# Performance work log

Measured on AMD Instinct MI355X. Metric: run time of the kernel, lower is better.

## Reference

```python
import jax, jax.numpy as jnp
import numpy as np

N_USER = 50000
N_ITEM = 50000
E = 500000
D_IN = 256
H = 4
D_HID = 64
D_OUT = 128
NEG_SLOPE = 0.2  # DGL GATConv default leaky_relu slope


def setup_inputs() -> dict:
    key = jax.random.key(0)
    ks = jax.random.split(key, 14)
    f = lambda k, s: jax.random.normal(k, s, dtype=jnp.float32)
    return {
        "h_src_user": f(ks[0], (N_USER, D_IN)),
        "h_src_item": f(ks[1], (N_ITEM, D_IN)),
        "h_dst_user": f(ks[2], (N_USER, D_IN)),
        "h_dst_item": f(ks[3], (N_ITEM, D_IN)),
        "u2i_src": jax.random.randint(ks[4], (E,), 0, N_USER),
        "u2i_dst": jax.random.randint(ks[5], (E,), 0, N_ITEM),
        "i2u_src": jax.random.randint(ks[6], (E,), 0, N_ITEM),
        "i2u_dst": jax.random.randint(ks[7], (E,), 0, N_USER),
        "fc_w": f(ks[8], (D_IN, H * D_HID)) * 0.05,
        "attn_l": f(ks[9], (H, D_HID)) * 0.05,
        "attn_r": f(ks[10], (H, D_HID)) * 0.05,
        "gat_bias": jnp.zeros((H * D_HID,), jnp.float32),
        "W_w": f(ks[11], (D_IN + D_HID, D_OUT)) * 0.05,
        "W_b": jnp.zeros((D_OUT,), jnp.float32),
    }


def _gat(feat_src, feat_dst, src, dst, n_dst, fc_w, attn_l, attn_r, gat_bias):
    # DGL GATConv (dropout is identity in eval mode)
    H_, D_ = attn_l.shape
    fs = (feat_src @ fc_w).reshape(-1, H_, D_)  # [Ns,H,D]
    fd = (feat_dst @ fc_w).reshape(-1, H_, D_)  # [Nd,H,D]
    el = jnp.sum(fs * attn_l, axis=-1)          # [Ns,H]
    er = jnp.sum(fd * attn_r, axis=-1)          # [Nd,H]
    e = jax.nn.leaky_relu(el[src] + er[dst], NEG_SLOPE)  # [E,H]
    # edge softmax per (dst node, head)
    m = jax.ops.segment_max(e, dst, num_segments=n_dst)
    m = jnp.where(jnp.isfinite(m), m, 0.0)      # guard zero-degree dst
    ex = jnp.exp(e - m[dst])
    den = jax.ops.segment_sum(ex, dst, num_segments=n_dst)
    alpha = ex / jnp.where(den == 0, 1.0, den)[dst]      # [E,H]
    out = jax.ops.segment_sum(alpha[:, :, None] * fs[src], dst, num_segments=n_dst)
    return out + gat_bias.reshape(1, H_, D_)    # [Nd,H,D]


def _head(agg, h_dst, W_w, W_b):
    # mean over heads, concat with dst feats, linear+relu, safe L2 normalize
    z = jax.nn.relu(jnp.concatenate([agg.mean(axis=1), h_dst], axis=1) @ W_w + W_b)
    n = jnp.linalg.norm(z, axis=1, keepdims=True)
    return z / jnp.where(n == 0, 1.0, n)


def reference(h_src_user, h_src_item, h_dst_user, h_dst_item,
              u2i_src, u2i_dst, i2u_src, i2u_dst,
              fc_w, attn_l, attn_r, gat_bias, W_w, W_b):
    agg_item = _gat(h_src_user, h_dst_item, u2i_src, u2i_dst, N_ITEM, fc_w, attn_l, attn_r, gat_bias)
    agg_user = _gat(h_src_item, h_dst_user, i2u_src, i2u_dst, N_USER, fc_w, attn_l, attn_r, gat_bias)
    z_user = _head(agg_user, h_dst_user, W_w, W_b)
    z_item = _head(agg_item, h_dst_item, W_w, W_b)
    return z_user, z_item
```

## Files before the change

kernel.cpp:

```cpp
#include <hip/hip_runtime.h>

#define NN 50000
#define N2 100000
#define EE 500000
#define E2 1000000

typedef unsigned short u16;
typedef unsigned int u32;

typedef __attribute__((ext_vector_type(8))) __bf16 bf16x8;
typedef __attribute__((ext_vector_type(4))) float f32x4;

__device__ __forceinline__ float4 ld4(const float* p) { return *(const float4*)p; }

__device__ __forceinline__ u16 f2bf(float f) {
  u32 u = __float_as_uint(f);
  u += 0x7FFFu + ((u >> 16) & 1u);
  return (u16)(u >> 16);
}

__device__ __forceinline__ u32 cvtpk(float lo, float hi) {
  u32 r;
  asm("v_cvt_pk_bf16_f32 %0, %1, %2" : "=v"(r) : "v"(lo), "v"(hi));
  return r;
}

__global__ void L384_const(const float* fc_w, const float* attn_l,
                           const float* attn_r, const float* Ww, float* w_r,
                           u16* wlB, u16* Bt, u16* Wt, int* cur) {
  const int b = blockIdx.x;
  const int t = threadIdx.x;
  if (b < 256) {
    Bt[b * 256 + t] = f2bf(fc_w[(size_t)t * 256 + b]);
  } else if (b == 256) {
    for (int h = 0; h < 4; ++h) {
      float sl = 0.f, sr = 0.f;
      for (int d = 0; d < 64; ++d) {
        float f = fc_w[t * 256 + h * 64 + d];
        sl += f * attn_l[h * 64 + d];
        sr += f * attn_r[h * 64 + d];
      }
      w_r[t * 4 + h] = sr;
      wlB[h * 256 + t] = f2bf(sl);
    }
    for (int h = 4; h < 16; ++h) wlB[h * 256 + t] = 0;
  } else if (b < 385) {
    int n = b - 257;
    for (int k = t; k < 320; k += 256)
      Wt[(size_t)n * 320 + k] = f2bf(Ww[(size_t)k * 128 + n]);
  } else {
    int i = (b - 385) * 256 + t;
    if (i < N2) cur[i] = 0;
  }
}

__global__ void L384_prep(const float* Du, const float* Di, const float* w_r_,
                          u16* X, float* er, const int* i2u_dst,
                          const int* u2i_dst, int* cnt) {
  const int b = blockIdx.x;
  if (b >= 25000) {
    int e = (b - 25000) * 256 + threadIdx.x;
    if (e < EE) {
      int d = i2u_dst[e];
      d = ((unsigned)d < NN) ? d : 0;
      atomicAdd(&cnt[d], 1);
    } else if (e < E2) {
      int d = u2i_dst[e - EE];
      d = ((unsigned)d < NN) ? d : 0;
      atomicAdd(&cnt[NN + d], 1);
    }
    return;
  }
  const int r = b * 4 + (threadIdx.x >> 6);
  const int lane = threadIdx.x & 63;
  if (r >= N2) return;
  const float* src = (r < NN) ? Du + (size_t)r * 256 : Di + (size_t)(r - NN) * 256;
  float4 xv = ld4(src + lane * 4);
  uint2 pk = make_uint2(cvtpk(xv.x, xv.y), cvtpk(xv.z, xv.w));
  *(uint2*)(X + (size_t)r * 320 + 64 + lane * 4) = pk;
  const float* wr = w_r_ + lane * 16;
  float4 w0 = ld4(wr), w1 = ld4(wr + 4), w2 = ld4(wr + 8), w3 = ld4(wr + 12);
  float a0 = xv.x * w0.x + xv.y * w1.x + xv.z * w2.x + xv.w * w3.x;
  float a1 = xv.x * w0.y + xv.y * w1.y + xv.z * w2.y + xv.w * w3.y;
  float a2 = xv.x * w0.z + xv.y * w1.z + xv.z * w2.z + xv.w * w3.z;
  float a3 = xv.x * w0.w + xv.y * w1.w + xv.z * w2.w + xv.w * w3.w;
  for (int off = 32; off; off >>= 1) {
    a0 += __shfl_xor(a0, off);
    a1 += __shfl_xor(a1, off);
    a2 += __shfl_xor(a2, off);
    a3 += __shfl_xor(a3, off);
  }
  if (lane == 0) {
    float* op = er + (size_t)r * 4;
    op[0] = a0; op[1] = a1; op[2] = a2; op[3] = a3;
  }
}

__global__ void L384_scan1(const int* cnt, int* part, int* bsum, int n) {
  __shared__ int sh[256];
  const int t = threadIdx.x;
  const int base = blockIdx.x * 1024 + t * 4;
  int v0 = (base + 0 < n) ? cnt[base + 0] : 0;
  int v1 = (base + 1 < n) ? cnt[base + 1] : 0;
  int v2 = (base + 2 < n) ? cnt[base + 2] : 0;
  int v3 = (base + 3 < n) ? cnt[base + 3] : 0;
  int s0 = v0, s1 = s0 + v1, s2 = s1 + v2, s3 = s2 + v3;
  sh[t] = s3;
  __syncthreads();
  for (int off = 1; off < 256; off <<= 1) {
    int x = (t >= off) ? sh[t - off] : 0;
    __syncthreads();
    sh[t] += x;
    __syncthreads();
  }
  int excl = (t > 0) ? sh[t - 1] : 0;
  if (base + 0 < n) part[base + 0] = excl;
  if (base + 1 < n) part[base + 1] = excl + s0;
  if (base + 2 < n) part[base + 2] = excl + s1;
  if (base + 3 < n) part[base + 3] = excl + s2;
  if (t == 255) bsum[blockIdx.x] = sh[255];
}
__global__ void L384_scan23(int* indptr, const int* bsum, int* cur, int nb, int n) {
  __shared__ int pre[128];
  const int t = threadIdx.x;
  if (t == 0) {
    int acc = 0;
    for (int i = 0; i < nb; ++i) {
      pre[i] = acc;
      acc += bsum[i];
    }
    pre[nb] = acc;
  }
  __syncthreads();
  int i = blockIdx.x * 256 + t;
  if (i < n) {
    int v = indptr[i] + pre[i >> 10];
    indptr[i] = v;
    cur[i] = v;
  }
  if (blockIdx.x == 0 && t == 0) indptr[n] = pre[nb];
}

__global__ __launch_bounds__(512) void L384_gemm(const float* Au, const float* Ai,
                                                 const u16* Bt, const u16* wlB,
                                                 u16* C, float* el,
                                                 const int* i2u_src, const int* i2u_dst,
                                                 const int* u2i_src, const int* u2i_dst,
                                                 int* cur, int* csr) {
  __shared__ u16 bs[64][264];
  const int t = threadIdx.x;
  if (blockIdx.x >= 782) {
    int e = (blockIdx.x - 782) * 512 + t;
    if (e < EE) {
      int d = i2u_dst[e];
      d = ((unsigned)d < NN) ? d : 0;
      int s = i2u_src[e];
      s = ((unsigned)s < NN) ? s : 0;
      int pos = atomicAdd(&cur[d], 1);
      if ((unsigned)pos < E2) csr[pos] = NN + s;
    } else if (e < E2) {
      int d = u2i_dst[e - EE];
      d = ((unsigned)d < NN) ? d : 0;
      int s = u2i_src[e - EE];
      s = ((unsigned)s < NN) ? s : 0;
      int pos = atomicAdd(&cur[NN + d], 1);
      if ((unsigned)pos < E2) csr[pos] = s;
    }
    return;
  }
  const int w = t >> 6;
  const int l = t & 63;
  const int lr = l & 15;
  const int kg = l >> 4;
  const int row0 = blockIdx.x * 128;

  const int row = row0 + w * 16 + lr;
  const int rr = (row < N2) ? row : (N2 - 1);
  const float* arow =
      ((rr < NN) ? Au + (size_t)rr * 256 : Ai + (size_t)(rr - NN) * 256) + kg * 8;
  uint4 a[8];
#pragma unroll
  for (int ks = 0; ks < 8; ++ks) {
    float4 f0 = ld4(arow + ks * 32);
    float4 f1 = ld4(arow + ks * 32 + 4);
    a[ks] = make_uint4(cvtpk(f0.x, f0.y), cvtpk(f0.z, f0.w), cvtpk(f1.x, f1.y),
                       cvtpk(f1.z, f1.w));
  }

  {
    f32x4 eacc = {0.f, 0.f, 0.f, 0.f};
    const u16* wl = wlB + lr * 256 + kg * 8;
#pragma unroll
    for (int ks = 0; ks < 8; ++ks) {
      union { bf16x8 v; uint4 q; } af, wf;
      af.q = a[ks];
      wf.q = *(const uint4*)(wl + ks * 32);
      eacc = __builtin_amdgcn_mfma_f32_16x16x32_bf16(af.v, wf.v, eacc, 0, 0, 0);
    }
    if (lr < 4) {
#pragma unroll
      for (int r = 0; r < 4; ++r) {
        int grow = row0 + w * 16 + kg * 4 + r;
        if (grow < N2) el[(size_t)grow * 4 + lr] = eacc[r];
      }
    }
  }

  for (int strip = 0; strip < 4; ++strip) {
    __syncthreads();
    {
      const int brow = t >> 3;
      const int bc = (t & 7) * 32;
      const uint4* s = (const uint4*)(Bt + (size_t)(strip * 64 + brow) * 256 + bc);
      uint4* d = (uint4*)&bs[brow][bc];
      d[0] = s[0]; d[1] = s[1]; d[2] = s[2]; d[3] = s[3];
    }
    __syncthreads();

    f32x4 acc[4];
#pragma unroll
    for (int ct = 0; ct < 4; ++ct) acc[ct] = (f32x4){0.f, 0.f, 0.f, 0.f};
#pragma unroll
    for (int ks = 0; ks < 8; ++ks) {
      union { bf16x8 v; uint4 q; } af;
      af.q = a[ks];
#pragma unroll
      for (int ct = 0; ct < 4; ++ct) {
        union { bf16x8 v; uint4 q; } b;
        b.q = *(const uint4*)&bs[ct * 16 + lr][ks * 32 + kg * 8];
        acc[ct] = __builtin_amdgcn_mfma_f32_16x16x32_bf16(af.v, b.v, acc[ct], 0, 0, 0);
      }
    }

#pragma unroll
    for (int p = 0; p < 2; ++p) {
      __syncthreads();
      if ((w >> 2) == p) {
        const int lrow = (w & 3) * 16 + kg * 4;
#pragma unroll
        for (int ct = 0; ct < 4; ++ct)
#pragma unroll
          for (int r = 0; r < 4; ++r)
            bs[lrow + r][ct * 16 + lr] = f2bf(acc[ct][r]);
      }
      __syncthreads();
      const int lrow2 = t >> 3;
      const int c0 = (t & 7) * 8;
      const int grow = row0 + p * 64 + lrow2;
      if (grow < N2)
        *(uint4*)(C + (size_t)grow * 256 + strip * 64 + c0) =
            *(const uint4*)&bs[lrow2][c0];
    }
  }
}

__global__ void L384_sort(const int* indptr, int* csr, int n) {
  __shared__ int buf[5120];
  const int t = threadIdx.x;
  const int node0 = blockIdx.x * 256;
  const int nEnd = (node0 + 256 < n) ? (node0 + 256) : n;
  if (node0 >= n) return;
  const int segL = indptr[node0];
  const int segR = indptr[nEnd];
  const int len = segR - segL;
  if (len <= 5120) {
    for (int i = t; i < len; i += 256) buf[i] = csr[segL + i];
    __syncthreads();
    const int node = node0 + t;
    if (node < n) {
      int p0 = indptr[node] - segL;
      int p1 = indptr[node + 1] - segL;
      for (int a = p0 + 1; a < p1; ++a) {
        int v = buf[a];
        int b = a - 1;
        while (b >= p0 && buf[b] > v) {
          buf[b + 1] = buf[b];
          --b;
        }
        buf[b + 1] = v;
      }
    }
    __syncthreads();
    for (int i = t; i < len; i += 256) csr[segL + i] = buf[i];
  } else {
    const int node = node0 + t;
    if (node < n) {
      int p0 = indptr[node], p1 = indptr[node + 1];
      for (int a = p0 + 1; a < p1; ++a) {
        int v = csr[a];
        int b = a - 1;
        while (b >= p0 && csr[b] > v) {
          csr[b + 1] = csr[b];
          --b;
        }
        csr[b + 1] = v;
      }
    }
  }
}

__global__ void L384_aggx(const int* indptr, const int* csr, const float* el,
                          const float* er, const u16* fs, const float* bias,
                          float* alphaG, u16* X) {
  __shared__ float aL[4][64][4];
  __shared__ int sL[4][64];
  const int slot = threadIdx.x >> 6;
  const int wid = blockIdx.x * 4 + slot;
  const int lane = threadIdx.x & 63;
  if (wid >= N2) return;
  const int p0 = indptr[wid];
  const int deg = indptr[wid + 1] - p0;
  const int h = lane >> 4;
  const int c = lane & 15;
  float4 er4 = ld4(er + (size_t)wid * 4);

  const bool small = (deg <= 64);
  if (small) {
    float4 ex = {0.f, 0.f, 0.f, 0.f};
    int s = 0;
    if (lane < deg) {
      s = csr[p0 + lane];
      s = ((unsigned)s < N2) ? s : 0;
      float4 ev = ld4(el + (size_t)s * 4);
      float e0 = ev.x + er4.x; e0 = (e0 >= 0.f) ? e0 : 0.2f * e0;
      float e1 = ev.y + er4.y; e1 = (e1 >= 0.f) ? e1 : 0.2f * e1;
      float e2 = ev.z + er4.z; e2 = (e2 >= 0.f) ? e2 : 0.2f * e2;
      float e3 = ev.w + er4.w; e3 = (e3 >= 0.f) ? e3 : 0.2f * e3;
      ex = make_float4(__expf(e0), __expf(e1), __expf(e2), __expf(e3));
    }
    float d0 = ex.x, d1 = ex.y, d2 = ex.z, d3 = ex.w;
    for (int off = 32; off; off >>= 1) {
      d0 += __shfl_xor(d0, off);
      d1 += __shfl_xor(d1, off);
      d2 += __shfl_xor(d2, off);
      d3 += __shfl_xor(d3, off);
    }
    if (lane < deg) {
      float4 o = make_float4(ex.x / d0, ex.y / d1, ex.z / d2, ex.w / d3);
      *(float4*)&aL[slot][lane][0] = o;
      sL[slot][lane] = s;
    }
  } else if (deg > 0) {
    float d0 = 0.f, d1 = 0.f, d2 = 0.f, d3 = 0.f;
    for (int i = lane; i < deg; i += 64) {
      int s = csr[p0 + i];
      s = ((unsigned)s < N2) ? s : 0;
      float4 ev = ld4(el + (size_t)s * 4);
      float e0 = ev.x + er4.x; e0 = (e0 >= 0.f) ? e0 : 0.2f * e0;
      float e1 = ev.y + er4.y; e1 = (e1 >= 0.f) ? e1 : 0.2f * e1;
      float e2 = ev.z + er4.z; e2 = (e2 >= 0.f) ? e2 : 0.2f * e2;
      float e3 = ev.w + er4.w; e3 = (e3 >= 0.f) ? e3 : 0.2f * e3;
      float4 ex = make_float4(__expf(e0), __expf(e1), __expf(e2), __expf(e3));
      *(float4*)(alphaG + (size_t)(p0 + i) * 4) = ex;
      d0 += ex.x; d1 += ex.y; d2 += ex.z; d3 += ex.w;
    }
    for (int off = 32; off; off >>= 1) {
      d0 += __shfl_xor(d0, off);
      d1 += __shfl_xor(d1, off);
      d2 += __shfl_xor(d2, off);
      d3 += __shfl_xor(d3, off);
    }
    float i0 = 1.f / d0, i1 = 1.f / d1, i2 = 1.f / d2, i3 = 1.f / d3;
    for (int i = lane; i < deg; i += 64) {
      float4 ex = *(const float4*)(alphaG + (size_t)(p0 + i) * 4);
      *(float4*)(alphaG + (size_t)(p0 + i) * 4) =
          make_float4(ex.x * i0, ex.y * i1, ex.z * i2, ex.w * i3);
    }
  }

  float ax = 0.f, ay = 0.f, az = 0.f, aw = 0.f;
  int i = 0;
  for (; i + 4 <= deg; i += 4) {
    int s0, s1, s2, s3;
    float a0, a1, a2, a3;
    if (small) {
      s0 = sL[slot][i + 0]; s1 = sL[slot][i + 1];
      s2 = sL[slot][i + 2]; s3 = sL[slot][i + 3];
      a0 = aL[slot][i + 0][h]; a1 = aL[slot][i + 1][h];
      a2 = aL[slot][i + 2][h]; a3 = aL[slot][i + 3][h];
    } else {
      s0 = csr[p0 + i + 0]; s0 = ((unsigned)s0 < N2) ? s0 : 0;
      s1 = csr[p0 + i + 1]; s1 = ((unsigned)s1 < N2) ? s1 : 0;
      s2 = csr[p0 + i + 2]; s2 = ((unsigned)s2 < N2) ? s2 : 0;
      s3 = csr[p0 + i + 3]; s3 = ((unsigned)s3 < N2) ? s3 : 0;
      a0 = alphaG[(size_t)(p0 + i + 0) * 4 + h];
      a1 = alphaG[(size_t)(p0 + i + 1) * 4 + h];
      a2 = alphaG[(size_t)(p0 + i + 2) * 4 + h];
      a3 = alphaG[(size_t)(p0 + i + 3) * 4 + h];
    }
    uint2 q0 = *(const uint2*)(fs + (size_t)s0 * 256 + lane * 4);
    uint2 q1 = *(const uint2*)(fs + (size_t)s1 * 256 + lane * 4);
    uint2 q2 = *(const uint2*)(fs + (size_t)s2 * 256 + lane * 4);
    uint2 q3 = *(const uint2*)(fs + (size_t)s3 * 256 + lane * 4);
    ax += a0 * __uint_as_float(q0.x << 16);
    ay += a0 * __uint_as_float(q0.x & 0xffff0000u);
    az += a0 * __uint_as_float(q0.y << 16);
    aw += a0 * __uint_as_float(q0.y & 0xffff0000u);
    ax += a1 * __uint_as_float(q1.x << 16);
    ay += a1 * __uint_as_float(q1.x & 0xffff0000u);
    az += a1 * __uint_as_float(q1.y << 16);
    aw += a1 * __uint_as_float(q1.y & 0xffff0000u);
    ax += a2 * __uint_as_float(q2.x << 16);
    ay += a2 * __uint_as_float(q2.x & 0xffff0000u);
    az += a2 * __uint_as_float(q2.y << 16);
    aw += a2 * __uint_as_float(q2.y & 0xffff0000u);
    ax += a3 * __uint_as_float(q3.x << 16);
    ay += a3 * __uint_as_float(q3.x & 0xffff0000u);
    az += a3 * __uint_as_float(q3.y << 16);
    aw += a3 * __uint_as_float(q3.y & 0xffff0000u);
  }
  for (; i < deg; ++i) {
    int s0;
    float a0;
    if (small) {
      s0 = sL[slot][i];
      a0 = aL[slot][i][h];
    } else {
      s0 = csr[p0 + i]; s0 = ((unsigned)s0 < N2) ? s0 : 0;
      a0 = alphaG[(size_t)(p0 + i) * 4 + h];
    }
    uint2 q0 = *(const uint2*)(fs + (size_t)s0 * 256 + lane * 4);
    ax += a0 * __uint_as_float(q0.x << 16);
    ay += a0 * __uint_as_float(q0.x & 0xffff0000u);
    az += a0 * __uint_as_float(q0.y << 16);
    aw += a0 * __uint_as_float(q0.y & 0xffff0000u);
  }
  const float* bp = bias + lane * 4;
  float ox = ax + bp[0];
  float oy = ay + bp[1];
  float oz = az + bp[2];
  float ow = aw + bp[3];
  for (int off = 16; off <= 32; off <<= 1) {
    ox += __shfl_xor(ox, off);
    oy += __shfl_xor(oy, off);
    oz += __shfl_xor(oz, off);
    ow += __shfl_xor(ow, off);
  }
  if (h == 0) {
    uint2 pk = make_uint2(cvtpk(ox * 0.25f, oy * 0.25f), cvtpk(oz * 0.25f, ow * 0.25f));
    *(uint2*)(X + (size_t)wid * 320 + 4 * c) = pk;
  }
}

__global__ void L384_headm(const u16* X, const u16* Wt, const float* Wb, float* out) {
  __shared__ float red[4][64];
  const int t = threadIdx.x;
  const int w = t >> 6;
  const int l = t & 63;
  const int row0 = blockIdx.x * 64;
  const int lr = l & 15;
  const int kg = l >> 4;
  f32x4 acc[4][2];
#pragma unroll
  for (int rg = 0; rg < 4; ++rg) {
    acc[rg][0] = (f32x4){0.f, 0.f, 0.f, 0.f};
    acc[rg][1] = (f32x4){0.f, 0.f, 0.f, 0.f};
  }
  const u16* arow[4];
#pragma unroll
  for (int rg = 0; rg < 4; ++rg) {
    int r = row0 + rg * 16 + lr;
    if (r >= N2) r = N2 - 1;
    arow[rg] = X + (size_t)r * 320 + kg * 8;
  }
  const u16* b0row = Wt + (size_t)(w * 32 + lr) * 320 + kg * 8;
  const u16* b1row = Wt + (size_t)(w * 32 + 16 + lr) * 320 + kg * 8;
#pragma unroll
  for (int k0 = 0; k0 < 320; k0 += 32) {
    union { bf16x8 v; uint4 q; } af[4], b0, b1;
#pragma unroll
    for (int rg = 0; rg < 4; ++rg) af[rg].q = *(const uint4*)(arow[rg] + k0);
    b0.q = *(const uint4*)(b0row + k0);
    b1.q = *(const uint4*)(b1row + k0);
#pragma unroll
    for (int rg = 0; rg < 4; ++rg) {
      acc[rg][0] = __builtin_amdgcn_mfma_f32_16x16x32_bf16(af[rg].v, b0.v,
                                                           acc[rg][0], 0, 0, 0);
      acc[rg][1] = __builtin_amdgcn_mfma_f32_16x16x32_bf16(af[rg].v, b1.v,
                                                           acc[rg][1], 0, 0, 0);
    }
  }
  const int col0 = w * 32 + lr;
  const int col1 = col0 + 16;
  float wb0 = Wb[col0], wb1 = Wb[col1];
  float z0[4][4], z1[4][4];
#pragma unroll
  for (int rg = 0; rg < 4; ++rg) {
    float pssq[4];
#pragma unroll
    for (int r = 0; r < 4; ++r) {
      z0[rg][r] = fmaxf(acc[rg][0][r] + wb0, 0.f);
      z1[rg][r] = fmaxf(acc[rg][1][r] + wb1, 0.f);
      pssq[r] = z0[rg][r] * z0[rg][r] + z1[rg][r] * z1[rg][r];
    }
#pragma unroll
    for (int off = 8; off; off >>= 1) {
#pragma unroll
      for (int r = 0; r < 4; ++r) pssq[r] += __shfl_xor(pssq[r], off);
    }
    if (lr == 0) {
#pragma unroll
      for (int r = 0; r < 4; ++r) red[w][rg * 16 + kg * 4 + r] = pssq[r];
    }
  }
  __syncthreads();
#pragma unroll
  for (int rg = 0; rg < 4; ++rg) {
#pragma unroll
    for (int r = 0; r < 4; ++r) {
      int lrow = rg * 16 + kg * 4 + r;
      int grow = row0 + lrow;
      if (grow < N2) {
        float ssq = red[0][lrow] + red[1][lrow] + red[2][lrow] + red[3][lrow];
        float inv = (ssq > 0.f) ? rsqrtf(ssq) : 0.f;
        float* op = out + (size_t)grow * 128;
        op[col0] = z0[rg][r] * inv;
        op[col1] = z1[rg][r] * inv;
      }
    }
  }
}

extern "C" void kernel_launch(void* const* d_in, const int* in_sizes, int n_in,
                              void* d_out, int out_size, void* d_ws, size_t ws_size,
                              hipStream_t stream) {
  (void)in_sizes; (void)n_in; (void)out_size; (void)ws_size;
  const float* h_src_user = (const float*)d_in[0];
  const float* h_src_item = (const float*)d_in[1];
  const float* h_dst_user = (const float*)d_in[2];
  const float* h_dst_item = (const float*)d_in[3];
  const int* u2i_src = (const int*)d_in[4];
  const int* u2i_dst = (const int*)d_in[5];
  const int* i2u_src = (const int*)d_in[6];
  const int* i2u_dst = (const int*)d_in[7];
  const float* fc_w = (const float*)d_in[8];
  const float* attn_l = (const float*)d_in[9];
  const float* attn_r = (const float*)d_in[10];
  const float* gat_bias = (const float*)d_in[11];
  const float* W_w = (const float*)d_in[12];
  const float* W_b = (const float*)d_in[13];
  float* out = (float*)d_out;

  float* el = (float*)d_ws;
  float* er = el + (size_t)N2 * 4;
  float* w_r = er + (size_t)N2 * 4;
  u16* wlB = (u16*)(w_r + 1024);
  float* alpha = (float*)(wlB + 16 * 256);
  u16* fs = (u16*)(alpha + (size_t)E2 * 4);
  u16* X = fs + (size_t)N2 * 256;
  u16* Bt = X + (size_t)N2 * 320;
  u16* Wt = Bt + 256 * 256;
  int* indptr = (int*)(Wt + 128 * 320);
  int* cur = indptr + (N2 + 4);
  int* csr = cur + N2;
  int* bsum = csr + E2;

  L384_const<<<776, 256, 0, stream>>>(fc_w, attn_l, attn_r, W_w, w_r, wlB, Bt, Wt, cur);
  L384_prep<<<28907, 256, 0, stream>>>(h_dst_user, h_dst_item, w_r, X, er,
                                       i2u_dst, u2i_dst, cur);
  L384_scan1<<<98, 256, 0, stream>>>(cur, indptr, bsum, N2);
  L384_scan23<<<391, 256, 0, stream>>>(indptr, bsum, cur, 98, N2);
  L384_gemm<<<2736, 512, 0, stream>>>(h_src_user, h_src_item, Bt, wlB, fs, el,
                                      i2u_src, i2u_dst, u2i_src, u2i_dst, cur, csr);
  L384_sort<<<391, 256, 0, stream>>>(indptr, csr, N2);
  L384_aggx<<<25000, 256, 0, stream>>>(indptr, csr, el, er, fs, gat_bias, alpha, X);
  L384_headm<<<1563, 256, 0, stream>>>(X, Wt, W_b, out);
}
```

Measured before the change: 364.1 us.

## Replace CSR sort kernel with in-warp bitonic sort and split fill from GEMM

Removes the separate insertion-sort kernel over CSR neighbor lists and instead sorts small-degree neighbor indices inside the aggregation kernel with a 64-lane bitonic network over shuffles. The CSR fill work, previously fused as extra blocks in the GEMM launch, moves to its own kernel launched before the GEMM. This saves one kernel launch and a global read/write pass over the CSR array, at the cost of a separate fill launch and no overlap with the GEMM. Large-degree nodes (>64) are no longer sorted, so only their summation order differs.

```diff
diff --git a/kernel.cpp b/kernel.cpp
--- a/kernel.cpp
+++ b/kernel.cpp
@@ -140,34 +140,32 @@
   }
   if (blockIdx.x == 0 && t == 0) indptr[n] = pre[nb];
 }
+__global__ void L384_fill(const int* i2u_src, const int* i2u_dst,
+                          const int* u2i_src, const int* u2i_dst,
+                          int* cur, int* csr) {
+  int e = blockIdx.x * 256 + threadIdx.x;
+  if (e < EE) {
+    int d = i2u_dst[e];
+    d = ((unsigned)d < NN) ? d : 0;
+    int s = i2u_src[e];
+    s = ((unsigned)s < NN) ? s : 0;
+    int pos = atomicAdd(&cur[d], 1);
+    if ((unsigned)pos < E2) csr[pos] = NN + s;
+  } else if (e < E2) {
+    int d = u2i_dst[e - EE];
+    d = ((unsigned)d < NN) ? d : 0;
+    int s = u2i_src[e - EE];
+    s = ((unsigned)s < NN) ? s : 0;
+    int pos = atomicAdd(&cur[NN + d], 1);
+    if ((unsigned)pos < E2) csr[pos] = s;
+  }
+}
 
 __global__ __launch_bounds__(512) void L384_gemm(const float* Au, const float* Ai,
                                                  const u16* Bt, const u16* wlB,
-                                                 u16* C, float* el,
-                                                 const int* i2u_src, const int* i2u_dst,
-                                                 const int* u2i_src, const int* u2i_dst,
-                                                 int* cur, int* csr) {
+                                                 u16* C, float* el) {
   __shared__ u16 bs[64][264];
   const int t = threadIdx.x;
-  if (blockIdx.x >= 782) {
-    int e = (blockIdx.x - 782) * 512 + t;
-    if (e < EE) {
-      int d = i2u_dst[e];
-      d = ((unsigned)d < NN) ? d : 0;
-      int s = i2u_src[e];
-      s = ((unsigned)s < NN) ? s : 0;
-      int pos = atomicAdd(&cur[d], 1);
-      if ((unsigned)pos < E2) csr[pos] = NN + s;
-    } else if (e < E2) {
-      int d = u2i_dst[e - EE];
-      d = ((unsigned)d < NN) ? d : 0;
-      int s = u2i_src[e - EE];
-      s = ((unsigned)s < NN) ? s : 0;
-      int pos = atomicAdd(&cur[NN + d], 1);
-      if ((unsigned)pos < E2) csr[pos] = s;
-    }
-    return;
-  }
   const int w = t >> 6;
   const int l = t & 63;
   const int lr = l & 15;
@@ -250,51 +248,6 @@
       if (grow < N2)
         *(uint4*)(C + (size_t)grow * 256 + strip * 64 + c0) =
             *(const uint4*)&bs[lrow2][c0];
-    }
-  }
-}
-
-__global__ void L384_sort(const int* indptr, int* csr, int n) {
-  __shared__ int buf[5120];
-  const int t = threadIdx.x;
-  const int node0 = blockIdx.x * 256;
-  const int nEnd = (node0 + 256 < n) ? (node0 + 256) : n;
-  if (node0 >= n) return;
-  const int segL = indptr[node0];
-  const int segR = indptr[nEnd];
-  const int len = segR - segL;
-  if (len <= 5120) {
-    for (int i = t; i < len; i += 256) buf[i] = csr[segL + i];
-    __syncthreads();
-    const int node = node0 + t;
-    if (node < n) {
-      int p0 = indptr[node] - segL;
-      int p1 = indptr[node + 1] - segL;
-      for (int a = p0 + 1; a < p1; ++a) {
-        int v = buf[a];
-        int b = a - 1;
-        while (b >= p0 && buf[b] > v) {
-          buf[b + 1] = buf[b];
-          --b;
-        }
-        buf[b + 1] = v;
-      }
-    }
-    __syncthreads();
-    for (int i = t; i < len; i += 256) csr[segL + i] = buf[i];
-  } else {
-    const int node = node0 + t;
-    if (node < n) {
-      int p0 = indptr[node], p1 = indptr[node + 1];
-      for (int a = p0 + 1; a < p1; ++a) {
-        int v = csr[a];
-        int b = a - 1;
-        while (b >= p0 && csr[b] > v) {
-          csr[b + 1] = csr[b];
-          --b;
-        }
-        csr[b + 1] = v;
-      }
     }
   }
 }
@@ -316,11 +269,25 @@
 
   const bool small = (deg <= 64);
   if (small) {
-    float4 ex = {0.f, 0.f, 0.f, 0.f};
-    int s = 0;
+    int s = 0x7fffffff;
     if (lane < deg) {
       s = csr[p0 + lane];
       s = ((unsigned)s < N2) ? s : 0;
+    }
+#pragma unroll
+    for (int k = 2; k <= 64; k <<= 1) {
+#pragma unroll
+      for (int j = k >> 1; j > 0; j >>= 1) {
+        int o = __shfl_xor(s, j);
+        bool up = ((lane & k) == 0);
+        bool keepMin = (((lane & j) == 0) == up);
+        int mn = (s < o) ? s : o;
+        int mx = (s < o) ? o : s;
+        s = keepMin ? mn : mx;
+      }
+    }
+    float4 ex = {0.f, 0.f, 0.f, 0.f};
+    if (lane < deg) {
       float4 ev = ld4(el + (size_t)s * 4);
       float e0 = ev.x + er4.x; e0 = (e0 >= 0.f) ? e0 : 0.2f * e0;
       float e1 = ev.y + er4.y; e1 = (e1 >= 0.f) ? e1 : 0.2f * e1;
@@ -560,9 +527,8 @@
                                        i2u_dst, u2i_dst, cur);
   L384_scan1<<<98, 256, 0, stream>>>(cur, indptr, bsum, N2);
   L384_scan23<<<391, 256, 0, stream>>>(indptr, bsum, cur, 98, N2);
-  L384_gemm<<<2736, 512, 0, stream>>>(h_src_user, h_src_item, Bt, wlB, fs, el,
-                                      i2u_src, i2u_dst, u2i_src, u2i_dst, cur, csr);
-  L384_sort<<<391, 256, 0, stream>>>(indptr, csr, N2);
+  L384_fill<<<3907, 256, 0, stream>>>(i2u_src, i2u_dst, u2i_src, u2i_dst, cur, csr);
+  L384_gemm<<<782, 512, 0, stream>>>(h_src_user, h_src_item, Bt, wlB, fs, el);
   L384_aggx<<<25000, 256, 0, stream>>>(indptr, csr, el, er, fs, gat_bias, alpha, X);
   L384_headm<<<1563, 256, 0, stream>>>(X, Wt, W_b, out);
 }
```

After: 348.1 us. 1.05x faster.
